# Kernel optimization log

Measured on AMD Instinct MI355X. Metric: run time of the kernel, lower is better.

## Reference

```python
import jax, jax.numpy as jnp
import numpy as np

SMPL_PARENT = np.array([0,0,0,1,2,3,4,5,6,7,8,9,9,9,12,13,14,16,17,18,19,20,21], dtype=np.int64)

def quat2mat(quat):
    # quat: [N,4] (w,x,y,z) -> [N,3,3]
    q = quat / jnp.linalg.norm(quat, axis=1, keepdims=True)
    w, x, y, z = q[:, 0], q[:, 1], q[:, 2], q[:, 3]
    w2, x2, y2, z2 = w*w, x*x, y*y, z*z
    wx, wy, wz = w*x, w*y, w*z
    xy, xz, yz = x*y, x*z, y*z
    R = jnp.stack([w2+x2-y2-z2, 2*xy-2*wz, 2*wy+2*xz,
                   2*wz+2*xy, w2-x2+y2-z2, 2*yz-2*wx,
                   2*xz-2*wy, 2*wx+2*yz, w2-x2-y2+z2], axis=1)
    return R.reshape(-1, 3, 3)

def rodrigues(theta):
    # theta: [N,3] axis-angle -> [N,3,3]
    angle = jnp.linalg.norm(theta + 1e-8, axis=1, keepdims=True)
    normalized = theta / angle
    half = angle * 0.5
    quat = jnp.concatenate([jnp.cos(half), jnp.sin(half) * normalized], axis=1)
    return quat2mat(quat)

def setup_inputs() -> dict:
    key = jax.random.key(0)
    ks = jax.random.split(key, 8)
    B, V = 64, 50000
    pose = jax.random.normal(ks[0], (B, 72), dtype=jnp.float32) * 0.3
    beta = jax.random.normal(ks[1], (B, 300), dtype=jnp.float32) * 0.03
    v_template = jax.random.normal(ks[2], (V, 3), dtype=jnp.float32)
    shapedirs = jax.random.normal(ks[3], (V, 3, 300), dtype=jnp.float32) * 0.01
    posedirs = jax.random.normal(ks[4], (V, 3, 207), dtype=jnp.float32) * 0.01
    Jr = jax.random.uniform(ks[5], (24, V), dtype=jnp.float32)
    J_regressor = Jr / jnp.sum(Jr, axis=1, keepdims=True)
    w = jax.random.uniform(ks[6], (V, 24), dtype=jnp.float32)
    weights = w / jnp.sum(w, axis=1, keepdims=True)
    parent = jnp.asarray(SMPL_PARENT)
    return {"pose": pose, "beta": beta, "v_template": v_template,
            "shapedirs": shapedirs, "posedirs": posedirs,
            "J_regressor": J_regressor, "weights": weights, "parent": parent}

def reference(pose, beta, v_template, shapedirs, posedirs, J_regressor, weights, parent):
    B = pose.shape[0]
    parent_np = np.asarray(jax.device_get(parent))
    # shape blendshapes: [B,V,3]
    v_shaped = jnp.einsum('vds,bs->bvd', shapedirs, beta) + v_template[None]
    J = jnp.einsum('jv,bvd->bjd', J_regressor, v_shaped)
    # pose -> rotation matrices [B,24,3,3]
    R = rodrigues(pose.reshape(-1, 3)).reshape(B, 24, 3, 3)
    lrotmin = (R[:, 1:] - jnp.eye(3, dtype=R.dtype)).reshape(B, 207)
    # pose blendshapes
    v_posed = v_shaped + jnp.einsum('vdp,bp->bvd', posedirs, lrotmin)
    # relative joint locations
    J_rel = J.at[:, 1:].set(J[:, 1:] - J[:, parent_np])
    # local transforms [B,24,4,4]
    G_top = jnp.concatenate([R, J_rel[..., None]], axis=-1)  # [B,24,3,4]
    pad = jnp.broadcast_to(jnp.array([0., 0., 0., 1.], dtype=R.dtype), (B, 24, 1, 4))
    G_local = jnp.concatenate([G_top, pad], axis=2)
    # kinematic chain (24 structurally-distinct joints)
    Gs = [G_local[:, 0]]
    for i in range(1, 24):
        Gs.append(jnp.matmul(Gs[parent_np[i - 1]], G_local[:, i]))
    G = jnp.stack(Gs, axis=1)  # [B,24,4,4]
    # remove rest-pose translation: G[...,:,3] -= G @ [J,0]
    rest4 = jnp.concatenate([J, jnp.zeros((B, 24, 1), dtype=J.dtype)], axis=2)  # [B,24,4]
    corr = jnp.einsum('bjmn,bjn->bjm', G, rest4)
    G = G.at[..., :, 3].add(-corr)
    # LBS: per-vertex transform [B,V,4,4]
    T = jnp.einsum('vj,bjmn->bvmn', weights, G)
    v_h = jnp.concatenate([v_posed, jnp.ones_like(v_posed[..., :1])], axis=-1)  # [B,V,4]
    v = jnp.einsum('bvmn,bvn->bvm', T, v_h)[..., :3]
    return v
```

## Files before the change

### kernel.cpp

```cpp
#include <hip/hip_runtime.h>
#include <math.h>

#define NV 50000
#define NM 150000

typedef float  f32x4  __attribute__((ext_vector_type(4)));
typedef __bf16 bf16x8 __attribute__((ext_vector_type(8)));
typedef float  f4u    __attribute__((ext_vector_type(4), aligned(4)));

__constant__ int c_par[24]   = {0, 0,0,0, 1,2,3, 4,5,6, 7,8,9,9,9, 12,13,14, 16,17, 18,19, 20,21};
__constant__ int c_depth[24] = {0, 1,1,1, 2,2,2, 3,3,3, 4,4,4,4,4, 5,5,5, 6,6, 7,7, 8,8};

__global__ __launch_bounds__(256)
void prep_kernel(const float* __restrict__ beta, float* __restrict__ betaT,
                 float* __restrict__ J)
{
    int i = blockIdx.x * 256 + threadIdx.x;
    if (i < 300 * 64) {
        int k = i >> 6, b = i & 63;
        betaT[i] = beta[b * 300 + k];
    }
    if (i < 64 * 24 * 3) J[i] = 0.f;
}

template<int K, int MODE>
__global__ __launch_bounds__(512, 4)
void gemm_mfma(const float* __restrict__ A, const float* __restrict__ Bt,
               const float* __restrict__ add, float* __restrict__ C)
{
    constexpr int NFULL = K / 32;
    constexpr int KTAIL = K - NFULL * 32;
    constexpr int NC    = NFULL + 1;
    constexpr int PB    = NC * 32 + 8;
    __shared__ __bf16 Bs[64 * PB];

    const int t    = threadIdx.x;
    const int row0 = blockIdx.x * 128;
    const int w    = __builtin_amdgcn_readfirstlane(t >> 6);
    const int l    = t & 63;
    const int lr   = l & 15;
    const int kb   = l >> 4;

    constexpr int NTASK = 64 * NC * 4;
    #pragma unroll
    for (int s = 0; s < (NTASK + 511) / 512; ++s) {
        const int id = t + s * 512;
        if (id < NTASK) {
            const int n  = id & 63;
            const int k8 = (id >> 6) * 8;
            float v[8];
            #pragma unroll
            for (int e = 0; e < 8; ++e) {
                int k = k8 + e;
                v[e] = (k < K) ? Bt[(size_t)k * 64 + n] : 0.f;
            }
            bf16x8 bv;
            #pragma unroll
            for (int e = 0; e < 8; ++e) bv[e] = (__bf16)v[e];
            *(bf16x8*)(Bs + n * PB + k8) = bv;
        }
    }
    __syncthreads();

    if (row0 + w * 16 >= NM) return;
    const int grow = row0 + w * 16 + lr;
    const float* Arow = A + (size_t)grow * K;

    f4u a[2 * NC];
    #pragma unroll
    for (int c = 0; c < NFULL; ++c) {
        a[2*c]   = *(const f4u*)(Arow + c * 32 + kb * 8);
        a[2*c+1] = *(const f4u*)(Arow + c * 32 + kb * 8 + 4);
    }
    {
        float tv[8];
        #pragma unroll
        for (int e = 0; e < 8; ++e) {
            int k = NFULL * 32 + kb * 8 + e;
            tv[e] = (k < K) ? Arow[k] : 0.f;
        }
        a[2*NFULL]   = (f4u){tv[0], tv[1], tv[2], tv[3]};
        a[2*NFULL+1] = (f4u){tv[4], tv[5], tv[6], tv[7]};
    }

    f32x4 acc[4] = {};
    #pragma unroll
    for (int c = 0; c < NC; ++c) {
        bf16x8 af;
        #pragma unroll
        for (int e = 0; e < 4; ++e) {
            af[e]     = (__bf16)a[2*c][e];
            af[4 + e] = (__bf16)a[2*c+1][e];
        }
        #pragma unroll
        for (int n = 0; n < 4; ++n) {
            const bf16x8 bfv = *(const bf16x8*)(Bs + (n * 16 + lr) * PB + c * 32 + kb * 8);
            if constexpr (MODE == 0)
                acc[n] = __builtin_amdgcn_mfma_f32_16x16x32_bf16(af, bfv, acc[n], 0, 0, 0);
            else
                acc[n] = __builtin_amdgcn_mfma_f32_16x16x32_bf16(bfv, af, acc[n], 0, 0, 0);
        }
    }

    if constexpr (MODE == 0) {
        f4u ta = *(const f4u*)(add + row0 + w * 16 + kb * 4);
        #pragma unroll
        for (int n = 0; n < 4; ++n)
            #pragma unroll
            for (int r = 0; r < 4; ++r)
                C[(size_t)(row0 + w * 16 + kb * 4 + r) * 64 + n * 16 + lr] = acc[n][r] + ta[r];
    } else {
        const size_t vrow = row0 + w * 16 + lr;
        #pragma unroll
        for (int m = 0; m < 4; ++m) {
            f4u av = *(const f4u*)(add + vrow * 64 + m * 16 + kb * 4);
            #pragma unroll
            for (int r = 0; r < 4; ++r)
                C[(size_t)(m * 16 + kb * 4 + r) * NM + vrow] = acc[m][r] + av[r];
        }
    }
}

__global__ __launch_bounds__(512)
void jreduce_kernel(const float* __restrict__ vs, const float* __restrict__ Jr,
                    float* J)
{
    __shared__ float Ls[4][64][73];
    const int t = threadIdx.x;
    const int b = t & 63;
    const int w = __builtin_amdgcn_readfirstlane(t >> 6);

    float acc[24][3];
    #pragma unroll
    for (int j = 0; j < 24; ++j) { acc[j][0]=0.f; acc[j][1]=0.f; acc[j][2]=0.f; }

    const int v0 = blockIdx.x * 200 + w * 25;
    #pragma unroll 5
    for (int v = v0; v < v0 + 25; ++v) {
        float p0 = vs[(size_t)(v*3+0)*64 + b];
        float p1 = vs[(size_t)(v*3+1)*64 + b];
        float p2 = vs[(size_t)(v*3+2)*64 + b];
        #pragma unroll
        for (int j = 0; j < 24; ++j) {
            float r = Jr[(size_t)j*NV + v];
            acc[j][0] += r*p0; acc[j][1] += r*p1; acc[j][2] += r*p2;
        }
    }

    if (w < 4) {
        float* d = Ls[w][b];
        #pragma unroll
        for (int j = 0; j < 24; ++j) {
            d[j*3+0] = acc[j][0]; d[j*3+1] = acc[j][1]; d[j*3+2] = acc[j][2];
        }
    }
    __syncthreads();
    if (w >= 4) {
        float* d = Ls[w-4][b];
        #pragma unroll
        for (int j = 0; j < 24; ++j) {
            d[j*3+0] += acc[j][0]; d[j*3+1] += acc[j][1]; d[j*3+2] += acc[j][2];
        }
    }
    __syncthreads();

    #pragma unroll
    for (int q = 0; q < 9; ++q) {
        int oid = t * 9 + q;
        int bb = oid / 72, c = oid - bb * 72;
        float s = Ls[0][bb][c] + Ls[1][bb][c] + Ls[2][bb][c] + Ls[3][bb][c];
        atomicAdd(&J[(size_t)bb * 72 + c], s);
    }
}

__global__ __launch_bounds__(192)
void pose_kernel(const float* __restrict__ pose, const float* __restrict__ J,
                 float* __restrict__ G, float* __restrict__ lrotT)
{
    __shared__ float Gl[8][24][12];
    __shared__ float Gc[8][24][12];
    const int t  = threadIdx.x;
    const int bl = t / 24;
    const int j  = t % 24;
    const int b  = blockIdx.x * 8 + bl;

    float tx = pose[b*72 + j*3 + 0];
    float ty = pose[b*72 + j*3 + 1];
    float tz = pose[b*72 + j*3 + 2];
    float ax = tx + 1e-8f, ay = ty + 1e-8f, az = tz + 1e-8f;
    float angle = sqrtf(ax*ax + ay*ay + az*az);
    float nx = tx / angle, ny = ty / angle, nz = tz / angle;
    float half = 0.5f * angle;
    float sw = sinf(half);
    float qw = cosf(half), qx = sw*nx, qy = sw*ny, qz = sw*nz;
    float qn = sqrtf(qw*qw + qx*qx + qy*qy + qz*qz);
    qw /= qn; qx /= qn; qy /= qn; qz /= qn;
    float w2=qw*qw, x2=qx*qx, y2=qy*qy, z2=qz*qz;
    float xy=qx*qy, xz=qx*qz, yz=qy*qz, wx=qw*qx, wy=qw*qy, wz=qw*qz;
    float r00 = w2+x2-y2-z2, r01 = 2.f*(xy-wz), r02 = 2.f*(wy+xz);
    float r10 = 2.f*(wz+xy), r11 = w2-x2+y2-z2, r12 = 2.f*(yz-wx);
    float r20 = 2.f*(xz-wy), r21 = 2.f*(wx+yz), r22 = w2-x2-y2+z2;

    if (j >= 1) {
        const int k9 = (j-1)*9;
        lrotT[(size_t)(k9+0)*64+b]=r00-1.f; lrotT[(size_t)(k9+1)*64+b]=r01;
        lrotT[(size_t)(k9+2)*64+b]=r02;     lrotT[(size_t)(k9+3)*64+b]=r10;
        lrotT[(size_t)(k9+4)*64+b]=r11-1.f; lrotT[(size_t)(k9+5)*64+b]=r12;
        lrotT[(size_t)(k9+6)*64+b]=r20;     lrotT[(size_t)(k9+7)*64+b]=r21;
        lrotT[(size_t)(k9+8)*64+b]=r22-1.f;
    }
    float jx = J[(size_t)(b*24+j)*3+0];
    float jy = J[(size_t)(b*24+j)*3+1];
    float jz = J[(size_t)(b*24+j)*3+2];
    float rx = jx, ry = jy, rz = jz;
    if (j > 0) {
        int p = c_par[j];
        rx -= J[(size_t)(b*24+p)*3+0];
        ry -= J[(size_t)(b*24+p)*3+1];
        rz -= J[(size_t)(b*24+p)*3+2];
    }
    float* gl = Gl[bl][j];
    gl[0]=r00; gl[1]=r01; gl[2]=r02;  gl[3]=rx;
    gl[4]=r10; gl[5]=r11; gl[6]=r12;  gl[7]=ry;
    gl[8]=r20; gl[9]=r21; gl[10]=r22; gl[11]=rz;
    __syncthreads();

    if (j == 0) {
        #pragma unroll
        for (int c = 0; c < 12; ++c) Gc[bl][0][c] = Gl[bl][0][c];
    }
    const int dj = c_depth[j];
    for (int lvl = 1; lvl <= 8; ++lvl) {
        __syncthreads();
        if (dj == lvl) {
            const float* Aa = Gc[bl][c_par[j]];
            const float* Bb = Gl[bl][j];
            float* D = Gc[bl][j];
            #pragma unroll
            for (int r = 0; r < 3; ++r) {
                float a0=Aa[r*4+0], a1=Aa[r*4+1], a2=Aa[r*4+2], a3=Aa[r*4+3];
                D[r*4+0] = a0*Bb[0] + a1*Bb[4] + a2*Bb[8];
                D[r*4+1] = a0*Bb[1] + a1*Bb[5] + a2*Bb[9];
                D[r*4+2] = a0*Bb[2] + a1*Bb[6] + a2*Bb[10];
                D[r*4+3] = a0*Bb[3] + a1*Bb[7] + a2*Bb[11] + a3;
            }
        }
    }
    __syncthreads();

    const float* Gi = Gc[bl][j];
    float* go = G + (size_t)(b*24 + j) * 12;
    #pragma unroll
    for (int r = 0; r < 3; ++r) {
        go[r*4+0] = Gi[r*4+0];
        go[r*4+1] = Gi[r*4+1];
        go[r*4+2] = Gi[r*4+2];
        go[r*4+3] = Gi[r*4+3] - (Gi[r*4+0]*jx + Gi[r*4+1]*jy + Gi[r*4+2]*jz);
    }
}

__global__ __launch_bounds__(256)
void skin_kernel(const float* __restrict__ vp, const float* __restrict__ G,
                 const float* __restrict__ wts, float* __restrict__ out)
{
    const int v = blockIdx.x * 256 + threadIdx.x;
    if (v >= NV) return;
    const int b0 = blockIdx.y * 8;
    float w[24];
    const float4* wp = (const float4*)(wts + (size_t)v * 24);
    #pragma unroll
    for (int q = 0; q < 6; ++q) {
        float4 t = wp[q];
        w[q*4+0]=t.x; w[q*4+1]=t.y; w[q*4+2]=t.z; w[q*4+3]=t.w;
    }
    for (int b = b0; b < b0 + 8; ++b) {
        const float* pb = vp + (size_t)b * NM + v*3;
        float px = pb[0], py = pb[1], pz = pb[2];
        float ox = 0.f, oy = 0.f, oz = 0.f;
        const float* Gb = G + (size_t)b * 24 * 12;
        #pragma unroll
        for (int j = 0; j < 24; ++j) {
            const float* g = Gb + j*12;
            float wj = w[j];
            ox += wj * (g[0]*px + g[1]*py + g[2]*pz  + g[3]);
            oy += wj * (g[4]*px + g[5]*py + g[6]*pz  + g[7]);
            oz += wj * (g[8]*px + g[9]*py + g[10]*pz + g[11]);
        }
        float* ob = out + (size_t)b * NM + v*3;
        ob[0] = ox; ob[1] = oy; ob[2] = oz;
    }
}

extern "C" void kernel_launch(void* const* d_in, const int* in_sizes, int n_in,
                              void* d_out, int out_size, void* d_ws, size_t ws_size,
                              hipStream_t stream) {
    const float* pose       = (const float*)d_in[0];
    const float* beta       = (const float*)d_in[1];
    const float* v_template = (const float*)d_in[2];
    const float* shapedirs  = (const float*)d_in[3];
    const float* posedirs   = (const float*)d_in[4];
    const float* Jreg       = (const float*)d_in[5];
    const float* weights    = (const float*)d_in[6];
    float* out = (float*)d_out;

    char* ws = (char*)d_ws;
    float* vs_ws    = (float*)(ws);
    float* vp_ws    = (float*)(ws + 38400000);
    float* betaT_ws = (float*)(ws + 38400000);
    float* J_ws     = (float*)(ws + 76800000);
    float* G_ws     = (float*)(ws + 76818432);
    float* lrotT_ws = (float*)(ws + 76892160);

    prep_kernel<<<75, 256, 0, stream>>>(beta, betaT_ws, J_ws);
    gemm_mfma<300, 0><<<1172, 512, 0, stream>>>(shapedirs, betaT_ws, v_template, vs_ws);
    jreduce_kernel<<<250, 512, 0, stream>>>(vs_ws, Jreg, J_ws);
    pose_kernel<<<8, 192, 0, stream>>>(pose, J_ws, G_ws, lrotT_ws);
    gemm_mfma<207, 1><<<1172, 512, 0, stream>>>(posedirs, lrotT_ws, vs_ws, vp_ws);
    skin_kernel<<<dim3(196, 8), 256, 0, stream>>>(vp_ws, G_ws, weights, out);
}
```

Measured before the change: 572.1 us.

## Fuse pose-blendshape GEMM with skinning and ring-buffer A loads

Merges the posedirs GEMM and the LBS skinning into one kernel. The posed vertices stay in shared memory and are consumed directly for skinning, so the 38 MB vp intermediate never makes a global-memory round trip and one launch disappears. Each block now covers 126 rows (42 vertices) so its vertices are complete, and the A-operand loads in both GEMMs switch from loading every chunk up front to a 4-deep ring buffer to cut register pressure. As a cost, skinning runs on only 42 of 64 lanes per wave, and the extra shared memory may lower occupancy.

```diff
diff --git a/kernel.cpp b/kernel.cpp
--- a/kernel.cpp
+++ b/kernel.cpp
@@ -10,6 +10,22 @@
 
 __constant__ int c_par[24]   = {0, 0,0,0, 1,2,3, 4,5,6, 7,8,9,9,9, 12,13,14, 16,17, 18,19, 20,21};
 __constant__ int c_depth[24] = {0, 1,1,1, 2,2,2, 3,3,3, 4,4,4,4,4, 5,5,5, 6,6, 7,7, 8,8};
+
+#define LOAD_CHUNK(slot, cc) do {                                          \
+    if ((cc) < NFULL) {                                                    \
+        abuf[slot][0] = *(const f4u*)(Arow + (cc)*32 + kb*8);              \
+        abuf[slot][1] = *(const f4u*)(Arow + (cc)*32 + kb*8 + 4);          \
+    } else {                                                               \
+        float tv[8];                                                       \
+        _Pragma("unroll")                                                  \
+        for (int e = 0; e < 8; ++e) {                                      \
+            int kk = (cc)*32 + kb*8 + e;                                   \
+            tv[e] = (kk < K) ? Arow[kk] : 0.f;                             \
+        }                                                                  \
+        abuf[slot][0] = (f4u){tv[0],tv[1],tv[2],tv[3]};                    \
+        abuf[slot][1] = (f4u){tv[4],tv[5],tv[6],tv[7]};                    \
+    }                                                                      \
+} while (0)
 
 __global__ __launch_bounds__(256)
 void prep_kernel(const float* __restrict__ beta, float* __restrict__ betaT,
@@ -23,13 +39,12 @@
     if (i < 64 * 24 * 3) J[i] = 0.f;
 }
 
-template<int K, int MODE>
+template<int K>
 __global__ __launch_bounds__(512, 4)
 void gemm_mfma(const float* __restrict__ A, const float* __restrict__ Bt,
                const float* __restrict__ add, float* __restrict__ C)
 {
     constexpr int NFULL = K / 32;
-    constexpr int KTAIL = K - NFULL * 32;
     constexpr int NC    = NFULL + 1;
     constexpr int PB    = NC * 32 + 8;
     __shared__ __bf16 Bs[64 * PB];
@@ -48,15 +63,12 @@
         if (id < NTASK) {
             const int n  = id & 63;
             const int k8 = (id >> 6) * 8;
-            float v[8];
+            bf16x8 bv;
             #pragma unroll
             for (int e = 0; e < 8; ++e) {
                 int k = k8 + e;
-                v[e] = (k < K) ? Bt[(size_t)k * 64 + n] : 0.f;
-            }
-            bf16x8 bv;
-            #pragma unroll
-            for (int e = 0; e < 8; ++e) bv[e] = (__bf16)v[e];
+                bv[e] = (__bf16)((k < K) ? Bt[(size_t)k * 64 + n] : 0.f);
+            }
             *(bf16x8*)(Bs + n * PB + k8) = bv;
         }
     }
@@ -66,22 +78,9 @@
     const int grow = row0 + w * 16 + lr;
     const float* Arow = A + (size_t)grow * K;
 
-    f4u a[2 * NC];
-    #pragma unroll
-    for (int c = 0; c < NFULL; ++c) {
-        a[2*c]   = *(const f4u*)(Arow + c * 32 + kb * 8);
-        a[2*c+1] = *(const f4u*)(Arow + c * 32 + kb * 8 + 4);
-    }
-    {
-        float tv[8];
-        #pragma unroll
-        for (int e = 0; e < 8; ++e) {
-            int k = NFULL * 32 + kb * 8 + e;
-            tv[e] = (k < K) ? Arow[k] : 0.f;
-        }
-        a[2*NFULL]   = (f4u){tv[0], tv[1], tv[2], tv[3]};
-        a[2*NFULL+1] = (f4u){tv[4], tv[5], tv[6], tv[7]};
-    }
+    f4u abuf[4][2];
+    #pragma unroll
+    for (int d = 0; d < 4; ++d) LOAD_CHUNK(d, d);
 
     f32x4 acc[4] = {};
     #pragma unroll
@@ -89,34 +88,132 @@
         bf16x8 af;
         #pragma unroll
         for (int e = 0; e < 4; ++e) {
-            af[e]     = (__bf16)a[2*c][e];
-            af[4 + e] = (__bf16)a[2*c+1][e];
+            af[e]     = (__bf16)abuf[c & 3][0][e];
+            af[4 + e] = (__bf16)abuf[c & 3][1][e];
         }
         #pragma unroll
         for (int n = 0; n < 4; ++n) {
             const bf16x8 bfv = *(const bf16x8*)(Bs + (n * 16 + lr) * PB + c * 32 + kb * 8);
-            if constexpr (MODE == 0)
-                acc[n] = __builtin_amdgcn_mfma_f32_16x16x32_bf16(af, bfv, acc[n], 0, 0, 0);
-            else
-                acc[n] = __builtin_amdgcn_mfma_f32_16x16x32_bf16(bfv, af, acc[n], 0, 0, 0);
-        }
-    }
-
-    if constexpr (MODE == 0) {
-        f4u ta = *(const f4u*)(add + row0 + w * 16 + kb * 4);
-        #pragma unroll
-        for (int n = 0; n < 4; ++n)
+            acc[n] = __builtin_amdgcn_mfma_f32_16x16x32_bf16(af, bfv, acc[n], 0, 0, 0);
+        }
+        if (c + 4 < NC) LOAD_CHUNK(c & 3, c + 4);
+    }
+
+    f4u ta = *(const f4u*)(add + row0 + w * 16 + kb * 4);
+    #pragma unroll
+    for (int n = 0; n < 4; ++n)
+        #pragma unroll
+        for (int r = 0; r < 4; ++r)
+            C[(size_t)(row0 + w * 16 + kb * 4 + r) * 64 + n * 16 + lr] = acc[n][r] + ta[r];
+}
+
+__global__ __launch_bounds__(512, 4)
+void posed_skin(const float* __restrict__ A, const float* __restrict__ Bt,
+                const float* __restrict__ vs, const float* __restrict__ G,
+                const float* __restrict__ wts, float* __restrict__ out)
+{
+    constexpr int K     = 207;
+    constexpr int NFULL = K / 32;
+    constexpr int NC    = NFULL + 1;
+    constexpr int PB    = NC * 32 + 8;
+    __shared__ __bf16 Bs[64 * PB];
+    __shared__ float  VP[128 * 67];
+
+    const int t    = threadIdx.x;
+    const int row0 = blockIdx.x * 126;
+    const int w    = __builtin_amdgcn_readfirstlane(t >> 6);
+    const int l    = t & 63;
+    const int lr   = l & 15;
+    const int kb   = l >> 4;
+
+    constexpr int NTASK = 64 * NC * 4;
+    #pragma unroll
+    for (int s = 0; s < (NTASK + 511) / 512; ++s) {
+        const int id = t + s * 512;
+        if (id < NTASK) {
+            const int n  = id & 63;
+            const int k8 = (id >> 6) * 8;
+            bf16x8 bv;
+            #pragma unroll
+            for (int e = 0; e < 8; ++e) {
+                int k = k8 + e;
+                bv[e] = (__bf16)((k < K) ? Bt[(size_t)k * 64 + n] : 0.f);
+            }
+            *(bf16x8*)(Bs + n * PB + k8) = bv;
+        }
+    }
+    __syncthreads();
+
+    const int grow = row0 + w * 16 + lr;
+    const int arow = grow < NM ? grow : NM - 1;
+    const float* Arow = A + (size_t)arow * K;
+
+    f4u abuf[4][2];
+    #pragma unroll
+    for (int d = 0; d < 4; ++d) LOAD_CHUNK(d, d);
+
+    f32x4 acc[4] = {};
+    #pragma unroll
+    for (int c = 0; c < NC; ++c) {
+        bf16x8 af;
+        #pragma unroll
+        for (int e = 0; e < 4; ++e) {
+            af[e]     = (__bf16)abuf[c & 3][0][e];
+            af[4 + e] = (__bf16)abuf[c & 3][1][e];
+        }
+        #pragma unroll
+        for (int m = 0; m < 4; ++m) {
+            const bf16x8 bfv = *(const bf16x8*)(Bs + (m * 16 + lr) * PB + c * 32 + kb * 8);
+            acc[m] = __builtin_amdgcn_mfma_f32_16x16x32_bf16(bfv, af, acc[m], 0, 0, 0);
+        }
+        if (c + 4 < NC) LOAD_CHUNK(c & 3, c + 4);
+    }
+
+    {
+        const int lrow = w * 16 + lr;
+        const float* av = vs + (size_t)arow * 64;
+        #pragma unroll
+        for (int m = 0; m < 4; ++m) {
+            f4u a4 = *(const f4u*)(av + m * 16 + kb * 4);
             #pragma unroll
             for (int r = 0; r < 4; ++r)
-                C[(size_t)(row0 + w * 16 + kb * 4 + r) * 64 + n * 16 + lr] = acc[n][r] + ta[r];
-    } else {
-        const size_t vrow = row0 + w * 16 + lr;
-        #pragma unroll
-        for (int m = 0; m < 4; ++m) {
-            f4u av = *(const f4u*)(add + vrow * 64 + m * 16 + kb * 4);
-            #pragma unroll
-            for (int r = 0; r < 4; ++r)
-                C[(size_t)(m * 16 + kb * 4 + r) * NM + vrow] = acc[m][r] + av[r];
+                VP[lrow * 67 + m * 16 + kb * 4 + r] = acc[m][r] + a4[r];
+        }
+    }
+    __syncthreads();
+
+    const int vl = l;
+    if (vl < 42) {
+        const int v = row0 / 3 + vl;
+        if (v < NV) {
+            float wj[24];
+            const f4u* wp = (const f4u*)(wts + (size_t)v * 24);
+            #pragma unroll
+            for (int q = 0; q < 6; ++q) {
+                f4u tw = wp[q];
+                wj[q*4+0]=tw[0]; wj[q*4+1]=tw[1]; wj[q*4+2]=tw[2]; wj[q*4+3]=tw[3];
+            }
+            const float px_ = VP[(3*vl+0)*67 + 0];
+            (void)px_;
+            #pragma unroll
+            for (int bi = 0; bi < 8; ++bi) {
+                const int b = w * 8 + bi;
+                float px = VP[(3*vl+0)*67 + b];
+                float py = VP[(3*vl+1)*67 + b];
+                float pz = VP[(3*vl+2)*67 + b];
+                float ox=0.f, oy=0.f, oz=0.f;
+                const float* Gb = G + (size_t)b * 24 * 12;
+                #pragma unroll
+                for (int j = 0; j < 24; ++j) {
+                    const float* g = Gb + j*12;
+                    float wjj = wj[j];
+                    ox += wjj * (g[0]*px + g[1]*py + g[2]*pz  + g[3]);
+                    oy += wjj * (g[4]*px + g[5]*py + g[6]*pz  + g[7]);
+                    oz += wjj * (g[8]*px + g[9]*py + g[10]*pz + g[11]);
+                }
+                float* ob = out + (size_t)b * NM + (size_t)v * 3;
+                ob[0] = ox; ob[1] = oy; ob[2] = oz;
+            }
         }
     }
 }
@@ -259,38 +356,6 @@
     }
 }
 
-__global__ __launch_bounds__(256)
-void skin_kernel(const float* __restrict__ vp, const float* __restrict__ G,
-                 const float* __restrict__ wts, float* __restrict__ out)
-{
-    const int v = blockIdx.x * 256 + threadIdx.x;
-    if (v >= NV) return;
-    const int b0 = blockIdx.y * 8;
-    float w[24];
-    const float4* wp = (const float4*)(wts + (size_t)v * 24);
-    #pragma unroll
-    for (int q = 0; q < 6; ++q) {
-        float4 t = wp[q];
-        w[q*4+0]=t.x; w[q*4+1]=t.y; w[q*4+2]=t.z; w[q*4+3]=t.w;
-    }
-    for (int b = b0; b < b0 + 8; ++b) {
-        const float* pb = vp + (size_t)b * NM + v*3;
-        float px = pb[0], py = pb[1], pz = pb[2];
-        float ox = 0.f, oy = 0.f, oz = 0.f;
-        const float* Gb = G + (size_t)b * 24 * 12;
-        #pragma unroll
-        for (int j = 0; j < 24; ++j) {
-            const float* g = Gb + j*12;
-            float wj = w[j];
-            ox += wj * (g[0]*px + g[1]*py + g[2]*pz  + g[3]);
-            oy += wj * (g[4]*px + g[5]*py + g[6]*pz  + g[7]);
-            oz += wj * (g[8]*px + g[9]*py + g[10]*pz + g[11]);
-        }
-        float* ob = out + (size_t)b * NM + v*3;
-        ob[0] = ox; ob[1] = oy; ob[2] = oz;
-    }
-}
-
 extern "C" void kernel_launch(void* const* d_in, const int* in_sizes, int n_in,
                               void* d_out, int out_size, void* d_ws, size_t ws_size,
                               hipStream_t stream) {
@@ -305,16 +370,14 @@
 
     char* ws = (char*)d_ws;
     float* vs_ws    = (float*)(ws);
-    float* vp_ws    = (float*)(ws + 38400000);
     float* betaT_ws = (float*)(ws + 38400000);
     float* J_ws     = (float*)(ws + 76800000);
     float* G_ws     = (float*)(ws + 76818432);
     float* lrotT_ws = (float*)(ws + 76892160);
 
     prep_kernel<<<75, 256, 0, stream>>>(beta, betaT_ws, J_ws);
-    gemm_mfma<300, 0><<<1172, 512, 0, stream>>>(shapedirs, betaT_ws, v_template, vs_ws);
+    gemm_mfma<300><<<1172, 512, 0, stream>>>(shapedirs, betaT_ws, v_template, vs_ws);
     jreduce_kernel<<<250, 512, 0, stream>>>(vs_ws, Jreg, J_ws);
     pose_kernel<<<8, 192, 0, stream>>>(pose, J_ws, G_ws, lrotT_ws);
-    gemm_mfma<207, 1><<<1172, 512, 0, stream>>>(posedirs, lrotT_ws, vs_ws, vp_ws);
-    skin_kernel<<<dim3(196, 8), 256, 0, stream>>>(vp_ws, G_ws, weights, out);
-}
+    posed_skin<<<1191, 512, 0, stream>>>(posedirs, lrotT_ws, vs_ws, G_ws, weights, out);
+}
```

Measured after the change: 586.7 us. 2.5% more time.
